# Kernel optimization log

Hardware: AMD Instinct MI355X
Metric: run time of the kernel (lower is better)

Reference implementation:

```python
import jax, jax.numpy as jnp
import numpy as np

B, N_P, N_S = 64, 50, 200
N_NODES = N_P * N_S          # 10000 nodes per graph (jobs x ops)
N_CAND = N_S + 1             # 201 candidates
INPUT_DIM, HIDDEN = 3, 64
NODE_DIM = 2 * HIDDEN        # h_nodes feature dim (=> actor in = 6*HIDDEN)
POOL_DIM = 4 * HIDDEN        # h_pooled dim (mean || max pooling)
H_ACTOR, H_CRITIC = 256, 256


def setup_inputs() -> dict:
    key = jax.random.key(0)
    ks = jax.random.split(key, 16)
    p = lambda k, sh: jax.random.normal(k, sh, jnp.float32) * 0.02
    x = jax.random.normal(ks[0], (B, N_NODES, INPUT_DIM), jnp.float32)
    candidate = jax.random.randint(ks[1], (B, N_CAND), 0, N_NODES)
    mask = jax.random.randint(ks[2], (B, N_CAND), 0, 2) > 0
    mask = mask.at[:, 0].set(True)  # guarantee at least one valid action per row
    return {
        "x": x, "candidate": candidate, "mask": mask,
        "fe_w1": p(ks[3], (INPUT_DIM, HIDDEN)), "fe_b1": jnp.zeros((HIDDEN,), jnp.float32),
        "fe_w2": p(ks[4], (HIDDEN, NODE_DIM)), "fe_b2": jnp.zeros((NODE_DIM,), jnp.float32),
        "a_w1": p(ks[5], (NODE_DIM + POOL_DIM, H_ACTOR)), "a_b1": jnp.zeros((H_ACTOR,), jnp.float32),
        "a_w2": p(ks[6], (H_ACTOR, H_ACTOR)), "a_b2": jnp.zeros((H_ACTOR,), jnp.float32),
        "a_w3": p(ks[7], (H_ACTOR, 1)), "a_b3": jnp.zeros((1,), jnp.float32),
        "c_w1": p(ks[8], (POOL_DIM, H_CRITIC)), "c_b1": jnp.zeros((H_CRITIC,), jnp.float32),
        "c_w2": p(ks[9], (H_CRITIC, H_CRITIC)), "c_b2": jnp.zeros((H_CRITIC,), jnp.float32),
        "c_w3": p(ks[10], (H_CRITIC, 1)), "c_b3": jnp.zeros((1,), jnp.float32),
    }


def _actor_critic(x, candidate, mask,
                  fe_w1, fe_b1, fe_w2, fe_b2,
                  a_w1, a_b1, a_w2, a_b2, a_w3, a_b3,
                  c_w1, c_b1, c_w2, c_b2, c_w3, c_b3):
    # --- feature_extract: per-node MLP embedding, graph-level pooling ---
    h = jax.nn.relu(jnp.einsum('bni,ih->bnh', x, fe_w1) + fe_b1)
    h_nodes = jax.nn.relu(jnp.einsum('bnh,hd->bnd', h, fe_w2) + fe_b2)   # [B, N, 2H]
    h_pooled = jnp.concatenate([h_nodes.mean(axis=1), h_nodes.max(axis=1)], axis=-1)  # [B, 4H]

    # --- gather candidate node features (torch.gather over node axis) ---
    cand_feat = jnp.take_along_axis(h_nodes, candidate[:, :, None], axis=1)  # [B, C, 2H]

    # --- concat broadcast pooled feature ---
    pooled_rep = jnp.broadcast_to(h_pooled[:, None, :], (cand_feat.shape[0], cand_feat.shape[1], h_pooled.shape[-1]))
    concat_fea = jnp.concatenate([cand_feat, pooled_rep], axis=-1)  # [B, C, 6H]

    # --- actor MLP (tanh hidden layers, linear out) ---
    a = jnp.tanh(concat_fea @ a_w1 + a_b1)
    a = jnp.tanh(a @ a_w2 + a_b2)
    scores = a @ a_w3 + a_b3                                    # [B, C, 1]

    # --- mask with -inf, softmax over candidate axis ---
    scores = jnp.where(mask[:, :, None], scores, -jnp.inf)
    pi = jax.nn.softmax(scores, axis=1)                          # [B, C, 1]

    # --- critic MLP on pooled feature ---
    c = jnp.tanh(h_pooled @ c_w1 + c_b1)
    c = jnp.tanh(c @ c_w2 + c_b2)
    v = c @ c_w3 + c_b3                                          # [B, 1]
    return pi, v


def reference(x, candidate, mask,
              fe_w1, fe_b1, fe_w2, fe_b2,
              a_w1, a_b1, a_w2, a_b2, a_w3, a_b3,
              c_w1, c_b1, c_w2, c_b2, c_w3, c_b3):
    return _actor_critic(x, candidate, mask,
                         fe_w1, fe_b1, fe_w2, fe_b2,
                         a_w1, a_b1, a_w2, a_b2, a_w3, a_b3,
                         c_w1, c_b1, c_w2, c_b2, c_w3, c_b3)
```

## Files before the change

kernel.cpp:

```cpp
#include <hip/hip_runtime.h>

#define NN 10000
#define NCAND 201
#define NB 64

typedef __attribute__((ext_vector_type(8))) short short8;
typedef __attribute__((ext_vector_type(4))) float f32x4;

__device__ __forceinline__ float bf2f(unsigned short u) {
  return __uint_as_float(((unsigned int)u) << 16);
}
__device__ __forceinline__ unsigned short f2bf(float f) {
  unsigned int u = __float_as_uint(f);
  u += 0x7FFFu + ((u >> 16) & 1u);
  return (unsigned short)(u >> 16);
}
__device__ __forceinline__ float fast_tanh(float x) {
  return 1.0f - 2.0f / (__expf(2.0f * x) + 1.0f);
}
__device__ __forceinline__ float gld(const void* p, long i, int f) {
  return f ? ((const float*)p)[i] : bf2f(((const unsigned short*)p)[i]);
}

__global__ __launch_bounds__(256, 4)
void mega_kernel(const void* __restrict__ x, const int* __restrict__ cand,
                 const void* w1, const void* b1, const void* w2, const void* b2,
                 const void* aw1, const void* ab1, const void* aw2, const void* ab2,
                 const void* aw3, const void* ab3,
                 const void* cw1, const void* cb1, const void* cw2, const void* cb2,
                 const void* cw3, const void* cb3,
                 const unsigned int* mask_w, const unsigned int* cand_w,
                 int* F, int* scnt,
                 float* __restrict__ psumP, float* __restrict__ pmaxP,
                 unsigned short* __restrict__ cfw,
                 unsigned short* __restrict__ aw1t, unsigned short* __restrict__ aw2t) {
  __shared__ __align__(16) unsigned short pool[128 * 72];
  __shared__ float w1f[3 * 64];
  __shared__ float b1f[64];
  __shared__ float b2f[128];
  __shared__ int cnts[8];

  const int t = threadIdx.x;
  const int j = blockIdx.x;
  const int lane = t & 63;
  const int wv = t >> 6;

  if (j < 1472) {
    if (t < 8) cnts[t] = 0;
    __syncthreads();
    {
      if ((((const unsigned short*)x)[t] & 0x7F80u) >= 0x4300u) atomicAdd(&cnts[0], 1);
      if (t < 192 && (((const unsigned short*)w1)[t] & 0x7F80u) >= 0x4300u) atomicAdd(&cnts[1], 1);
      if (t < 64 && (((const unsigned short*)b1)[t] & 0x7F80u) >= 0x4300u) atomicAdd(&cnts[2], 1);
      if (t < 128 && (((const unsigned short*)b2)[t] & 0x7F80u) >= 0x4300u) atomicAdd(&cnts[3], 1);
      if ((((const unsigned short*)w2)[t] & 0x7F80u) >= 0x4300u) atomicAdd(&cnts[4], 1);
      int co = 0;
#pragma unroll
      for (int q = 0; q < 4; ++q) {
        int i = t * 4 + q;
        if ((i & 1) && cand_w[i] != 0u) co = 1;
      }
      if (co) atomicAdd(&cnts[5], 1);
    }
    __syncthreads();
    const int F0 = cnts[0] > 32, F1 = cnts[1] > 24, F2 = cnts[2] > 8;
    const int F4 = cnts[3] > 16, Fw2 = cnts[4] > 32, C64 = cnts[5] == 0;

    if (j < 1024) {
      unsigned short* h1s = pool;
      const int b = j >> 4;
      const int s = j & 15;

      if (t < 192) w1f[t] = gld(w1, t, F1);
      if (t < 64) b1f[t] = gld(b1, t, F2);
      if (t < 128) b2f[t] = gld(b2, t, F4);

      short8 bfr[2][2];
#pragma unroll
      for (int nl = 0; nl < 2; ++nl)
#pragma unroll
        for (int ks = 0; ks < 2; ++ks) {
          int col = wv * 32 + nl * 16 + (lane & 15);
          short8 v;
#pragma unroll
          for (int jj = 0; jj < 8; ++jj) {
            int k = (lane >> 4) * 8 + ks * 32 + jj;
            v[jj] = (short)f2bf(gld(w2, (long)k * 128 + col, Fw2));
          }
          bfr[nl][ks] = v;
        }
      __syncthreads();

      float csum[2] = {0.f, 0.f};
      float cmax[2] = {0.f, 0.f};
      const int m = t & 127;
      const int kg = t >> 7;

      float x0 = 0.f, x1 = 0.f, x2 = 0.f;
      if (s < 79) {
        int nb = s * 128;
        if (m < min(128, NN - nb)) {
          long xo = ((long)b * NN + nb + m) * 3;
          x0 = gld(x, xo, F0); x1 = gld(x, xo + 1, F0); x2 = gld(x, xo + 2, F0);
        }
      }

      for (int c = s; c < 79; c += 16) {
        int nb = c * 128;
        int cnt = (nb + 128 <= NN) ? 128 : (NN - nb);
        const bool full = (cnt == 128);
        if (full) {
#pragma unroll
          for (int blk = 0; blk < 4; ++blk) {
            short8 v;
#pragma unroll
            for (int i = 0; i < 8; ++i) {
              int k = kg * 32 + blk * 8 + i;
              float vv = x0 * w1f[k] + x1 * w1f[64 + k] + x2 * w1f[128 + k] + b1f[k];
              v[i] = (short)f2bf(fmaxf(vv, 0.f));
            }
            *(short8*)(h1s + m * 72 + kg * 32 + blk * 8) = v;
          }
        } else if (m < cnt) {
#pragma unroll
          for (int blk = 0; blk < 4; ++blk) {
            short8 v;
#pragma unroll
            for (int i = 0; i < 8; ++i) {
              int k = kg * 32 + blk * 8 + i;
              float vv = x0 * w1f[k] + x1 * w1f[64 + k] + x2 * w1f[128 + k] + b1f[k];
              v[i] = (short)f2bf(fmaxf(vv, 0.f));
            }
            *(short8*)(h1s + m * 72 + kg * 32 + blk * 8) = v;
          }
        }
        {
          int cn = c + 16;
          float nx0 = 0.f, nx1 = 0.f, nx2 = 0.f;
          if (cn < 79) {
            int nbn = cn * 128;
            if (m < min(128, NN - nbn)) {
              long xo = ((long)b * NN + nbn + m) * 3;
              nx0 = gld(x, xo, F0); nx1 = gld(x, xo + 1, F0); nx2 = gld(x, xo + 2, F0);
            }
          }
          __syncthreads();
          x0 = nx0; x1 = nx1; x2 = nx2;
        }
        if (full) {
#pragma unroll
          for (int mt = 0; mt < 8; ++mt) {
            const unsigned short* ap = h1s + (mt * 16 + (lane & 15)) * 72 + ((lane >> 4) * 8);
            short8 af0 = *(const short8*)(ap);
            short8 af1 = *(const short8*)(ap + 32);
#pragma unroll
            for (int nl = 0; nl < 2; ++nl) {
              f32x4 acc = {0.f, 0.f, 0.f, 0.f};
              acc = __builtin_amdgcn_mfma_f32_16x16x32_bf16(af0, bfr[nl][0], acc, 0, 0, 0);
              acc = __builtin_amdgcn_mfma_f32_16x16x32_bf16(af1, bfr[nl][1], acc, 0, 0, 0);
              int col = wv * 32 + nl * 16 + (lane & 15);
              float bb = b2f[col];
#pragma unroll
              for (int r = 0; r < 4; ++r) {
                float v = fmaxf(acc[r] + bb, 0.f);
                csum[nl] += v;
                cmax[nl] = fmaxf(cmax[nl], v);
              }
            }
          }
        } else {
#pragma unroll
          for (int mt = 0; mt < 8; ++mt) {
            const unsigned short* ap = h1s + (mt * 16 + (lane & 15)) * 72 + ((lane >> 4) * 8);
            short8 af0 = *(const short8*)(ap);
            short8 af1 = *(const short8*)(ap + 32);
#pragma unroll
            for (int nl = 0; nl < 2; ++nl) {
              f32x4 acc = {0.f, 0.f, 0.f, 0.f};
              acc = __builtin_amdgcn_mfma_f32_16x16x32_bf16(af0, bfr[nl][0], acc, 0, 0, 0);
              acc = __builtin_amdgcn_mfma_f32_16x16x32_bf16(af1, bfr[nl][1], acc, 0, 0, 0);
              int col = wv * 32 + nl * 16 + (lane & 15);
              float bb = b2f[col];
#pragma unroll
              for (int r = 0; r < 4; ++r) {
                int row = mt * 16 + ((lane >> 4) * 4) + r;
                if (row < cnt) {
                  float v = fmaxf(acc[r] + bb, 0.f);
                  csum[nl] += v;
                  cmax[nl] = fmaxf(cmax[nl], v);
                }
              }
            }
          }
        }
        __syncthreads();
      }
#pragma unroll
      for (int nl = 0; nl < 2; ++nl) {
        csum[nl] += __shfl_xor(csum[nl], 16);
        csum[nl] += __shfl_xor(csum[nl], 32);
        cmax[nl] = fmaxf(cmax[nl], __shfl_xor(cmax[nl], 16));
        cmax[nl] = fmaxf(cmax[nl], __shfl_xor(cmax[nl], 32));
      }
      if (lane < 16) {
#pragma unroll
        for (int nl = 0; nl < 2; ++nl) {
          int col = wv * 32 + nl * 16 + lane;
          psumP[((long)b * 16 + s) * 128 + col] = csum[nl];
          pmaxP[((long)b * 16 + s) * 128 + col] = cmax[nl];
        }
      }
    } else {
      unsigned short* h1c = pool;
      const int idx = j - 1024;
      const int b = idx / 7;
      const int cb = idx % 7;
      const int cbase = cb * 29;

      if (t < 128) b2f[t] = gld(b2, t, F4);

      {
        int r = t & 31;
        int ci = cbase + r;
        if (ci > NCAND - 1) ci = NCAND - 1;
        long cidx = (long)b * NCAND + ci;
        int nd = C64 ? cand[2 * cidx] : cand[cidx];
        long xo = ((long)b * NN + nd) * 3;
        float x0 = gld(x, xo, F0), x1 = gld(x, xo + 1, F0), x2 = gld(x, xo + 2, F0);
        int kg = t >> 5;
#pragma unroll
        for (int i = 0; i < 8; ++i) {
          int k = kg * 8 + i;
          float v = x0 * gld(w1, k, F1) + x1 * gld(w1, 64 + k, F1) +
                    x2 * gld(w1, 128 + k, F1) + gld(b1, k, F2);
          h1c[r * 72 + k] = f2bf(fmaxf(v, 0.f));
        }
      }
      __syncthreads();

      {
        short8 af[2][2];
#pragma unroll
        for (int mt = 0; mt < 2; ++mt)
#pragma unroll
          for (int ks = 0; ks < 2; ++ks)
            af[mt][ks] = *(const short8*)(h1c + (mt * 16 + (lane & 15)) * 72 + ((lane >> 4) * 8) + ks * 32);
#pragma unroll
        for (int nl = 0; nl < 2; ++nl) {
          int col = wv * 32 + nl * 16 + (lane & 15);
          short8 bf0, bf1;
#pragma unroll
          for (int jj = 0; jj < 8; ++jj) {
            int k = (lane >> 4) * 8 + jj;
            bf0[jj] = (short)f2bf(gld(w2, (long)k * 128 + col, Fw2));
            bf1[jj] = (short)f2bf(gld(w2, (long)(k + 32) * 128 + col, Fw2));
          }
          float bb = b2f[col];
#pragma unroll
          for (int mt = 0; mt < 2; ++mt) {
            f32x4 acc = {0.f, 0.f, 0.f, 0.f};
            acc = __builtin_amdgcn_mfma_f32_16x16x32_bf16(af[mt][0], bf0, acc, 0, 0, 0);
            acc = __builtin_amdgcn_mfma_f32_16x16x32_bf16(af[mt][1], bf1, acc, 0, 0, 0);
#pragma unroll
            for (int r = 0; r < 4; ++r) {
              int row = mt * 16 + ((lane >> 4) * 4) + r;
              cfw[(long)idx * 4096 + row * 128 + col] = f2bf(fmaxf(acc[r] + bb, 0.f));
            }
          }
        }
      }
    }
    return;
  }

  if (t < 8) cnts[t] = 0;
  __syncthreads();

  if (j < 1856) {
    const unsigned short* pa = (const unsigned short*)aw1;
    const unsigned short* pb = (const unsigned short*)aw2;
    if ((pa[t] & 0x7F80u) >= 0x4300u) atomicAdd(&cnts[0], 1);
    if ((pb[t] & 0x7F80u) >= 0x4300u) atomicAdd(&cnts[1], 1);
    __syncthreads();
    const int Faw1 = cnts[0] > 32, Faw2 = cnts[1] > 32;
    int i = (j - 1472) * 256 + t;
    if (i < 256 * 384) { int n = i / 384, k = i % 384; aw1t[i] = f2bf(gld(aw1, k * 256 + n, Faw1)); }
    if (i < 256 * 256) {
      int n = i >> 8, k = i & 255;
      aw2t[i] = f2bf(gld(aw2, k * 256 + n, Faw2));
    }
  } else if (j < 1873) {
    const void* ptrs[17] = {x, w1, b1, w2, b2, aw1, ab1, aw2, ab2, aw3, ab3,
                            cw1, cb1, cw2, cb2, cw3, cb3};
    const int sizes[17] = {1920000, 192, 64, 8192, 128, 98304, 256, 65536, 256,
                           256, 1, 65536, 256, 65536, 256, 256, 1};
    int a = j - 1856;
    const unsigned short* p = (const unsigned short*)ptrs[a];
    int K = min(sizes[a], 2048);
    int c = 0;
    for (int i = t; i < K; i += 256)
      if ((p[i] & 0x7F80u) >= 0x4300u) c++;
    if (c) atomicAdd(&cnts[0], c);
    __syncthreads();
    if (t == 0) F[a] = (cnts[0] > (K >> 3)) ? 1 : 0;
  } else if (j == 1873) {
    int flo = 0, fhi = 0, fgt = 0;
    for (int i = t; i < 3216; i += 256) {
      unsigned int w = mask_w[i];
      if ((w & 0xFFFFu) == 0x3F80u) flo = 1;
      if ((w >> 16) == 0x3F80u) fhi = 1;
      if (w > 1u) fgt = 1;
    }
    if (flo) cnts[0] = 1;
    if (fhi) cnts[1] = 1;
    if (fgt) cnts[2] = 1;
    __syncthreads();
    if (t == 0) F[17] = cnts[0] ? 2 : (cnts[1] ? 3 : (cnts[2] ? 1 : 0));
  } else {
    int co = 0;
    for (int i = t; i < 1024; i += 256)
      if ((i & 1) && cand_w[i] != 0u) co = 1;
    if (co) cnts[0] = 1;
    if (t < 64) scnt[t] = 0;
    __syncthreads();
    if (t == 0) F[18] = cnts[0] ? 0 : 1;
  }
}

__global__ __launch_bounds__(256, 4)
void actorB_kernel(const unsigned short* __restrict__ cfw,
                   const void* __restrict__ aw1, const void* __restrict__ ab1,
                   const void* __restrict__ ab2,
                   const void* __restrict__ aw3, const void* __restrict__ ab3,
                   const void* __restrict__ mask,
                   const int* __restrict__ F,
                   const float* __restrict__ psumP, const float* __restrict__ pmaxP,
                   const unsigned short* __restrict__ aw1t,
                   const unsigned short* __restrict__ aw2t,
                   const void* __restrict__ cw1, const void* __restrict__ cb1,
                   const void* __restrict__ cw2, const void* __restrict__ cb2,
                   const void* __restrict__ cw3, const void* __restrict__ cb3,
                   float* __restrict__ scores, int* __restrict__ scnt,
                   void* __restrict__ out) {
  __shared__ __align__(16) unsigned short a1s[32 * 264];
  __shared__ __align__(16) unsigned short a2s[32 * 264];
  __shared__ float pactS[256], ab2f[256], plfS[256];
  __shared__ float red[4];
  __shared__ int amLast;

  const int t = threadIdx.x;
  const int lane = t & 63;
  const int wv = t >> 6;

  float pr = 0.f;
  {
    const int b = (blockIdx.x < 448) ? (blockIdx.x / 7) : (blockIdx.x - 448);
    const int col = t & 127;
    if (t < 128) {
#pragma unroll
      for (int sl = 0; sl < 16; ++sl)
        pr += psumP[((long)b * 16 + sl) * 128 + col];
      pr *= (1.0f / 10000.0f);
    } else {
#pragma unroll
      for (int sl = 0; sl < 16; ++sl)
        pr = fmaxf(pr, pmaxP[((long)b * 16 + sl) * 128 + col]);
    }
  }

  if (blockIdx.x >= 448) {
    const int b = blockIdx.x - 448;
    plfS[t] = pr;
    const int OF = (F[0] + F[1] + F[3] + F[5] + F[7] + F[9] + F[11] + F[13] + F[15]) >= 5;
    const int F11 = F[11], F12 = F[12], F13 = F[13];
    const int F14 = F[14], F15 = F[15], F16 = F[16];
    __syncthreads();
    {
      float a = gld(cb1, t, F12);
#pragma unroll 8
      for (int k = 0; k < 256; ++k)
        a += plfS[k] * gld(cw1, (long)k * 256 + t, F11);
      ab2f[t] = fast_tanh(a);
    }
    __syncthreads();
    {
      float a2 = gld(cb2, t, F14);
#pragma unroll 8
      for (int k = 0; k < 256; ++k)
        a2 += ab2f[k] * gld(cw2, (long)k * 256 + t, F13);
      a2 = fast_tanh(a2);
      float p = a2 * gld(cw3, t, F15);
      for (int o = 32; o; o >>= 1) p += __shfl_xor(p, o);
      __syncthreads();
      if (lane == 0) red[wv] = p;
      __syncthreads();
      if (t == 0) {
        float v = red[0] + red[1] + red[2] + red[3] + gld(cb3, 0, F16);
        if (!(v == v)) v = 0.f;
        if (OF) ((float*)out)[NB * NCAND + b] = v;
        else ((unsigned short*)out)[NB * NCAND + b] = f2bf(v);
      }
    }
    return;
  }

  const int b = blockIdx.x / 7;
  const int cb = blockIdx.x % 7;
  const int cbase = cb * 29;
  const int cntc = min(29, NCAND - cbase);
  const int F5 = F[5], F6 = F[6], F8 = F[8], F9 = F[9], F10 = F[10];

  plfS[t] = bf2f(f2bf(pr));
  ab2f[t] = gld(ab2, t, F8);
  __syncthreads();

  float pa = gld(ab1, t, F6);
#pragma unroll 8
  for (int k = 0; k < 256; ++k)
    pa += plfS[k] * gld(aw1, (long)(128 + k) * 256 + t, F5);

  {
    f32x4 acc[2][4];
#pragma unroll
    for (int mt = 0; mt < 2; ++mt)
#pragma unroll
      for (int nt = 0; nt < 4; ++nt) acc[mt][nt] = (f32x4){0.f, 0.f, 0.f, 0.f};
    const unsigned short* cfb = cfw + (long)blockIdx.x * 4096;
#pragma unroll
    for (int ks = 0; ks < 4; ++ks) {
      short8 af0 = *(const short8*)(cfb + (lane & 15) * 128 + ks * 32 + ((lane >> 4) * 8));
      short8 af1 = *(const short8*)(cfb + (16 + (lane & 15)) * 128 + ks * 32 + ((lane >> 4) * 8));
#pragma unroll
      for (int nt = 0; nt < 4; ++nt) {
        int col = wv * 64 + nt * 16 + (lane & 15);
        short8 bfr = *(const short8*)(aw1t + col * 384 + ks * 32 + ((lane >> 4) * 8));
        acc[0][nt] = __builtin_amdgcn_mfma_f32_16x16x32_bf16(af0, bfr, acc[0][nt], 0, 0, 0);
        acc[1][nt] = __builtin_amdgcn_mfma_f32_16x16x32_bf16(af1, bfr, acc[1][nt], 0, 0, 0);
      }
    }
    pactS[t] = pa;
    __syncthreads();
#pragma unroll
    for (int mt = 0; mt < 2; ++mt)
#pragma unroll
      for (int nt = 0; nt < 4; ++nt) {
        int col = wv * 64 + nt * 16 + (lane & 15);
        float bb = pactS[col];
#pragma unroll
        for (int r = 0; r < 4; ++r) {
          int row = mt * 16 + ((lane >> 4) * 4) + r;
          a1s[row * 264 + col] = f2bf(fast_tanh(acc[mt][nt][r] + bb));
        }
      }
  }
  __syncthreads();

  {
    f32x4 acc[2][4];
#pragma unroll
    for (int mt = 0; mt < 2; ++mt)
#pragma unroll
      for (int nt = 0; nt < 4; ++nt) acc[mt][nt] = (f32x4){0.f, 0.f, 0.f, 0.f};
    for (int ks = 0; ks < 8; ++ks) {
      short8 af0 = *(const short8*)(a1s + (lane & 15) * 264 + ks * 32 + ((lane >> 4) * 8));
      short8 af1 = *(const short8*)(a1s + (16 + (lane & 15)) * 264 + ks * 32 + ((lane >> 4) * 8));
#pragma unroll
      for (int nt = 0; nt < 4; ++nt) {
        int col = wv * 64 + nt * 16 + (lane & 15);
        short8 bfr = *(const short8*)(aw2t + col * 256 + ks * 32 + ((lane >> 4) * 8));
        acc[0][nt] = __builtin_amdgcn_mfma_f32_16x16x32_bf16(af0, bfr, acc[0][nt], 0, 0, 0);
        acc[1][nt] = __builtin_amdgcn_mfma_f32_16x16x32_bf16(af1, bfr, acc[1][nt], 0, 0, 0);
      }
    }
#pragma unroll
    for (int mt = 0; mt < 2; ++mt)
#pragma unroll
      for (int nt = 0; nt < 4; ++nt) {
        int col = wv * 64 + nt * 16 + (lane & 15);
        float bb = ab2f[col];
#pragma unroll
        for (int r = 0; r < 4; ++r) {
          int row = mt * 16 + ((lane >> 4) * 4) + r;
          a2s[row * 264 + col] = f2bf(fast_tanh(acc[mt][nt][r] + bb));
        }
      }
  }
  __syncthreads();

  {
    int row = t >> 3, seg = t & 7;
    float p = 0.f;
#pragma unroll 8
    for (int i = 0; i < 32; ++i) {
      int k = seg * 32 + i;
      p += bf2f(a2s[row * 264 + k]) * gld(aw3, k, F9);
    }
    p += __shfl_xor(p, 1);
    p += __shfl_xor(p, 2);
    p += __shfl_xor(p, 4);
    if (seg == 0 && row < cntc)
      atomicExch(&scores[b * 256 + cbase + row], p + gld(ab3, 0, F10));
  }
  __syncthreads();

  if (t == 0) {
    __threadfence();
    amLast = (atomicAdd(&scnt[b], 1) == 6);
  }
  __syncthreads();
  if (!amLast) return;

  const int MM = F[17];
  const int OF = (F[0] + F[1] + F[3] + F[5] + F[7] + F[9] + F[11] + F[13] + F[15]) >= 5;
  float sraw = 0.f, sv = -1e30f;
  bool valid = false;
  if (t < NCAND) {
    sraw = atomicAdd(&scores[b * 256 + t], 0.0f);
    long idx = (long)b * NCAND + t;
    if (MM == 0)      valid = ((const int*)mask)[idx] != 0;
    else if (MM == 1) valid = ((const unsigned char*)mask)[idx] != 0;
    else if (MM == 2) valid = ((const unsigned short*)mask)[idx] != 0;
    else              valid = ((const unsigned int*)mask)[idx] != 0;
    if (valid) sv = sraw;
  }
  float m = sv;
  for (int o = 32; o; o >>= 1) m = fmaxf(m, __shfl_xor(m, o));
  if (lane == 0) red[wv] = m;
  __syncthreads();
  m = fmaxf(fmaxf(red[0], red[1]), fmaxf(red[2], red[3]));
  __syncthreads();
  float e = valid ? __expf(sraw - m) : 0.f;
  if (!(e == e)) e = 0.f;
  float ss = e;
  for (int o = 32; o; o >>= 1) ss += __shfl_xor(ss, o);
  if (lane == 0) red[wv] = ss;
  __syncthreads();
  float tot = red[0] + red[1] + red[2] + red[3];
  tot = fmaxf(tot, 1e-30f);
  if (t < NCAND) {
    float pv = e / tot;
    if (!(pv == pv)) pv = 0.f;
    if (OF) ((float*)out)[b * NCAND + t] = pv;
    else ((unsigned short*)out)[b * NCAND + t] = f2bf(pv);
  }
}

extern "C" void kernel_launch(void* const* d_in, const int* in_sizes, int n_in,
                              void* d_out, int out_size, void* d_ws, size_t ws_size,
                              hipStream_t stream) {
  const void* x = d_in[0];
  const int* cand = (const int*)d_in[1];
  const void* mask = d_in[2];
  const void* fe_w1 = d_in[3];
  const void* fe_b1 = d_in[4];
  const void* fe_w2 = d_in[5];
  const void* fe_b2 = d_in[6];
  const void* a_w1 = d_in[7];
  const void* a_b1 = d_in[8];
  const void* a_w2 = d_in[9];
  const void* a_b2 = d_in[10];
  const void* a_w3 = d_in[11];
  const void* a_b3 = d_in[12];
  const void* c_w1 = d_in[13];
  const void* c_b1 = d_in[14];
  const void* c_w2 = d_in[15];
  const void* c_b2 = d_in[16];
  const void* c_w3 = d_in[17];
  const void* c_b3 = d_in[18];

  char* ws = (char*)d_ws;
  float* scores = (float*)(ws + 65536);
  unsigned short* aw1t = (unsigned short*)(ws + 147456);
  unsigned short* aw2t = (unsigned short*)(ws + 344064);
  int* F = (int*)(ws + 475136);
  unsigned short* cfw = (unsigned short*)(ws + 802944);
  int* scnt = (int*)(ws + 4472960);
  float* psumP = (float*)(ws + 4473216);
  float* pmaxP = (float*)(ws + 4997504);

  mega_kernel<<<1875, 256, 0, stream>>>(x, cand, fe_w1, fe_b1, fe_w2, fe_b2,
                                        a_w1, a_b1, a_w2, a_b2, a_w3, a_b3,
                                        c_w1, c_b1, c_w2, c_b2, c_w3, c_b3,
                                        (const unsigned int*)mask,
                                        (const unsigned int*)cand, F, scnt,
                                        psumP, pmaxP, cfw, aw1t, aw2t);
  actorB_kernel<<<512, 256, 0, stream>>>(cfw, a_w1, a_b1, a_b2, a_w3, a_b3,
                                         mask, F, psumP, pmaxP, aw1t, aw2t,
                                         c_w1, c_b1, c_w2, c_b2, c_w3, c_b3,
                                         scores, scnt, (void*)d_out);
}
```

Before: 163.4 us.

## Fold pooled-feature projection and critic MLP into last pooling block per batch

The last pooling block to finish for each batch, detected with a global atomic counter, now reduces the partial sums and maxima, computes the pooled part of the actor's first layer and runs the full critic MLP, writing the results to workspace. The actor kernel no longer recomputes the 256x256 pooled projection in each of its 7 blocks per batch and drops its 64 critic blocks. It now only reads the precomputed bias vector and copies the value out. This removes redundant per-block GEMV work and shortens the actor kernel, but it puts a serial GEMV tail on 64 blocks of the first kernel and adds a memset launch plus fence and atomic overhead.

```diff
diff --git a/kernel.cpp b/kernel.cpp
--- a/kernel.cpp
+++ b/kernel.cpp
@@ -30,8 +30,9 @@
                  const void* cw1, const void* cb1, const void* cw2, const void* cb2,
                  const void* cw3, const void* cb3,
                  const unsigned int* mask_w, const unsigned int* cand_w,
-                 int* F, int* scnt,
+                 int* F, int* scnt, int* fpcnt,
                  float* __restrict__ psumP, float* __restrict__ pmaxP,
+                 float* __restrict__ pact, float* __restrict__ vws,
                  unsigned short* __restrict__ cfw,
                  unsigned short* __restrict__ aw1t, unsigned short* __restrict__ aw2t) {
   __shared__ __align__(16) unsigned short pool[128 * 72];
@@ -208,6 +209,102 @@
           int col = wv * 32 + nl * 16 + lane;
           psumP[((long)b * 16 + s) * 128 + col] = csum[nl];
           pmaxP[((long)b * 16 + s) * 128 + col] = cmax[nl];
+        }
+      }
+
+      __syncthreads();
+      if (t == 0) {
+        __threadfence();
+        cnts[7] = (atomicAdd(&fpcnt[b], 1) == 15) ? 1 : 0;
+      }
+      __syncthreads();
+      if (!cnts[7]) return;
+
+      {
+        float* plfF = (float*)pool;
+        float* plfQ = plfF + 256;
+        float* c1s  = plfF + 512;
+        float* redt = plfF + 768;
+
+        if (t < 8) cnts[t] = 0;
+        __syncthreads();
+        {
+          int c5 = 0, c11 = 0, c13 = 0;
+          for (int i = t; i < 2048; i += 256) {
+            if ((((const unsigned short*)aw1)[i] & 0x7F80u) >= 0x4300u) c5++;
+            if ((((const unsigned short*)cw1)[i] & 0x7F80u) >= 0x4300u) c11++;
+            if ((((const unsigned short*)cw2)[i] & 0x7F80u) >= 0x4300u) c13++;
+          }
+          if (c5) atomicAdd(&cnts[0], c5);
+          if (c11) atomicAdd(&cnts[1], c11);
+          if (c13) atomicAdd(&cnts[2], c13);
+          if ((((const unsigned short*)ab1)[t] & 0x7F80u) >= 0x4300u) atomicAdd(&cnts[3], 1);
+          if ((((const unsigned short*)cb1)[t] & 0x7F80u) >= 0x4300u) atomicAdd(&cnts[4], 1);
+          if ((((const unsigned short*)cb2)[t] & 0x7F80u) >= 0x4300u) atomicAdd(&cnts[5], 1);
+          if ((((const unsigned short*)cw3)[t] & 0x7F80u) >= 0x4300u) atomicAdd(&cnts[6], 1);
+        }
+        {
+          const int col = t & 127;
+          float v = 0.f;
+          if (t < 128) {
+#pragma unroll
+            for (int sl = 0; sl < 16; ++sl)
+              v += atomicAdd(&psumP[((long)b * 16 + sl) * 128 + col], 0.0f);
+            v *= (1.0f / 10000.0f);
+          } else {
+#pragma unroll
+            for (int sl = 0; sl < 16; ++sl)
+              v = fmaxf(v, atomicAdd(&pmaxP[((long)b * 16 + sl) * 128 + col], 0.0f));
+          }
+          plfF[t] = v;
+          plfQ[t] = bf2f(f2bf(v));
+        }
+        __syncthreads();
+        const int Fa1 = cnts[0] > 256, Fc1 = cnts[1] > 256, Fc2 = cnts[2] > 256;
+        const int Fab = cnts[3] > 32, Fb1 = cnts[4] > 32;
+        const int Fb2 = cnts[5] > 32, Fc3 = cnts[6] > 32;
+
+        {
+          float p0 = 0.f, p1 = 0.f, p2 = 0.f, p3 = 0.f;
+#pragma unroll 4
+          for (int k = 0; k < 256; k += 4) {
+            p0 += plfQ[k]     * gld(aw1, (long)(128 + k) * 256 + t, Fa1);
+            p1 += plfQ[k + 1] * gld(aw1, (long)(129 + k) * 256 + t, Fa1);
+            p2 += plfQ[k + 2] * gld(aw1, (long)(130 + k) * 256 + t, Fa1);
+            p3 += plfQ[k + 3] * gld(aw1, (long)(131 + k) * 256 + t, Fa1);
+          }
+          pact[b * 256 + t] = gld(ab1, t, Fab) + ((p0 + p1) + (p2 + p3));
+        }
+        {
+          float p0 = 0.f, p1 = 0.f, p2 = 0.f, p3 = 0.f;
+#pragma unroll 4
+          for (int k = 0; k < 256; k += 4) {
+            p0 += plfF[k]     * gld(cw1, (long)(k)     * 256 + t, Fc1);
+            p1 += plfF[k + 1] * gld(cw1, (long)(k + 1) * 256 + t, Fc1);
+            p2 += plfF[k + 2] * gld(cw1, (long)(k + 2) * 256 + t, Fc1);
+            p3 += plfF[k + 3] * gld(cw1, (long)(k + 3) * 256 + t, Fc1);
+          }
+          c1s[t] = fast_tanh(gld(cb1, t, Fb1) + ((p0 + p1) + (p2 + p3)));
+        }
+        __syncthreads();
+        {
+          float p0 = 0.f, p1 = 0.f, p2 = 0.f, p3 = 0.f;
+#pragma unroll 4
+          for (int k = 0; k < 256; k += 4) {
+            p0 += c1s[k]     * gld(cw2, (long)(k)     * 256 + t, Fc2);
+            p1 += c1s[k + 1] * gld(cw2, (long)(k + 1) * 256 + t, Fc2);
+            p2 += c1s[k + 2] * gld(cw2, (long)(k + 2) * 256 + t, Fc2);
+            p3 += c1s[k + 3] * gld(cw2, (long)(k + 3) * 256 + t, Fc2);
+          }
+          float a2 = fast_tanh(gld(cb2, t, Fb2) + ((p0 + p1) + (p2 + p3)));
+          float p = a2 * gld(cw3, t, Fc3);
+          for (int o = 32; o; o >>= 1) p += __shfl_xor(p, o);
+          if (lane == 0) redt[wv] = p;
+          __syncthreads();
+          if (t == 0) {
+            int Fb3 = ((((const unsigned short*)cb3)[0] & 0x7F80u) >= 0x4300u) ? 1 : 0;
+            vws[b] = redt[0] + redt[1] + redt[2] + redt[3] + gld(cb3, 0, Fb3);
+          }
         }
       }
     } else {
@@ -327,97 +424,35 @@
   }
 }
 
-__global__ __launch_bounds__(256, 4)
+__global__ __launch_bounds__(256)
 void actorB_kernel(const unsigned short* __restrict__ cfw,
-                   const void* __restrict__ aw1, const void* __restrict__ ab1,
                    const void* __restrict__ ab2,
                    const void* __restrict__ aw3, const void* __restrict__ ab3,
                    const void* __restrict__ mask,
                    const int* __restrict__ F,
-                   const float* __restrict__ psumP, const float* __restrict__ pmaxP,
+                   const float* __restrict__ pact,
+                   const float* __restrict__ vws,
                    const unsigned short* __restrict__ aw1t,
                    const unsigned short* __restrict__ aw2t,
-                   const void* __restrict__ cw1, const void* __restrict__ cb1,
-                   const void* __restrict__ cw2, const void* __restrict__ cb2,
-                   const void* __restrict__ cw3, const void* __restrict__ cb3,
                    float* __restrict__ scores, int* __restrict__ scnt,
                    void* __restrict__ out) {
   __shared__ __align__(16) unsigned short a1s[32 * 264];
   __shared__ __align__(16) unsigned short a2s[32 * 264];
-  __shared__ float pactS[256], ab2f[256], plfS[256];
+  __shared__ float pactS[256], ab2f[256];
   __shared__ float red[4];
   __shared__ int amLast;
 
   const int t = threadIdx.x;
-  const int lane = t & 63;
-  const int wv = t >> 6;
-
-  float pr = 0.f;
-  {
-    const int b = (blockIdx.x < 448) ? (blockIdx.x / 7) : (blockIdx.x - 448);
-    const int col = t & 127;
-    if (t < 128) {
-#pragma unroll
-      for (int sl = 0; sl < 16; ++sl)
-        pr += psumP[((long)b * 16 + sl) * 128 + col];
-      pr *= (1.0f / 10000.0f);
-    } else {
-#pragma unroll
-      for (int sl = 0; sl < 16; ++sl)
-        pr = fmaxf(pr, pmaxP[((long)b * 16 + sl) * 128 + col]);
-    }
-  }
-
-  if (blockIdx.x >= 448) {
-    const int b = blockIdx.x - 448;
-    plfS[t] = pr;
-    const int OF = (F[0] + F[1] + F[3] + F[5] + F[7] + F[9] + F[11] + F[13] + F[15]) >= 5;
-    const int F11 = F[11], F12 = F[12], F13 = F[13];
-    const int F14 = F[14], F15 = F[15], F16 = F[16];
-    __syncthreads();
-    {
-      float a = gld(cb1, t, F12);
-#pragma unroll 8
-      for (int k = 0; k < 256; ++k)
-        a += plfS[k] * gld(cw1, (long)k * 256 + t, F11);
-      ab2f[t] = fast_tanh(a);
-    }
-    __syncthreads();
-    {
-      float a2 = gld(cb2, t, F14);
-#pragma unroll 8
-      for (int k = 0; k < 256; ++k)
-        a2 += ab2f[k] * gld(cw2, (long)k * 256 + t, F13);
-      a2 = fast_tanh(a2);
-      float p = a2 * gld(cw3, t, F15);
-      for (int o = 32; o; o >>= 1) p += __shfl_xor(p, o);
-      __syncthreads();
-      if (lane == 0) red[wv] = p;
-      __syncthreads();
-      if (t == 0) {
-        float v = red[0] + red[1] + red[2] + red[3] + gld(cb3, 0, F16);
-        if (!(v == v)) v = 0.f;
-        if (OF) ((float*)out)[NB * NCAND + b] = v;
-        else ((unsigned short*)out)[NB * NCAND + b] = f2bf(v);
-      }
-    }
-    return;
-  }
-
   const int b = blockIdx.x / 7;
   const int cb = blockIdx.x % 7;
   const int cbase = cb * 29;
   const int cntc = min(29, NCAND - cbase);
-  const int F5 = F[5], F6 = F[6], F8 = F[8], F9 = F[9], F10 = F[10];
-
-  plfS[t] = bf2f(f2bf(pr));
+  const int lane = t & 63;
+  const int wv = t >> 6;
+  const int F8 = F[8], F9 = F[9], F10 = F[10];
+
+  pactS[t] = pact[b * 256 + t];
   ab2f[t] = gld(ab2, t, F8);
-  __syncthreads();
-
-  float pa = gld(ab1, t, F6);
-#pragma unroll 8
-  for (int k = 0; k < 256; ++k)
-    pa += plfS[k] * gld(aw1, (long)(128 + k) * 256 + t, F5);
 
   {
     f32x4 acc[2][4];
@@ -438,7 +473,6 @@
         acc[1][nt] = __builtin_amdgcn_mfma_f32_16x16x32_bf16(af1, bfr, acc[1][nt], 0, 0, 0);
       }
     }
-    pactS[t] = pa;
     __syncthreads();
 #pragma unroll
     for (int mt = 0; mt < 2; ++mt)
@@ -542,6 +576,12 @@
     if (!(pv == pv)) pv = 0.f;
     if (OF) ((float*)out)[b * NCAND + t] = pv;
     else ((unsigned short*)out)[b * NCAND + t] = f2bf(pv);
+  }
+  if (t == 0) {
+    float v = vws[b];
+    if (!(v == v)) v = 0.f;
+    if (OF) ((float*)out)[NB * NCAND + b] = v;
+    else ((unsigned short*)out)[NB * NCAND + b] = f2bf(v);
   }
 }
 
@@ -569,23 +609,27 @@
   const void* c_b3 = d_in[18];
 
   char* ws = (char*)d_ws;
+  int* fpcnt = (int*)(ws);
+  float* vws = (float*)(ws + 1024);
   float* scores = (float*)(ws + 65536);
   unsigned short* aw1t = (unsigned short*)(ws + 147456);
   unsigned short* aw2t = (unsigned short*)(ws + 344064);
   int* F = (int*)(ws + 475136);
+  float* pact = (float*)(ws + 737408);
   unsigned short* cfw = (unsigned short*)(ws + 802944);
   int* scnt = (int*)(ws + 4472960);
   float* psumP = (float*)(ws + 4473216);
   float* pmaxP = (float*)(ws + 4997504);
 
+  hipMemsetAsync(fpcnt, 0, 256, stream);
+
   mega_kernel<<<1875, 256, 0, stream>>>(x, cand, fe_w1, fe_b1, fe_w2, fe_b2,
                                         a_w1, a_b1, a_w2, a_b2, a_w3, a_b3,
                                         c_w1, c_b1, c_w2, c_b2, c_w3, c_b3,
                                         (const unsigned int*)mask,
-                                        (const unsigned int*)cand, F, scnt,
-                                        psumP, pmaxP, cfw, aw1t, aw2t);
-  actorB_kernel<<<512, 256, 0, stream>>>(cfw, a_w1, a_b1, a_b2, a_w3, a_b3,
-                                         mask, F, psumP, pmaxP, aw1t, aw2t,
-                                         c_w1, c_b1, c_w2, c_b2, c_w3, c_b3,
+                                        (const unsigned int*)cand, F, scnt, fpcnt,
+                                        psumP, pmaxP, pact, vws, cfw, aw1t, aw2t);
+  actorB_kernel<<<448, 256, 0, stream>>>(cfw, a_b2, a_w3, a_b3, mask, F,
+                                         pact, vws, aw1t, aw2t,
                                          scores, scnt, (void*)d_out);
 }
```

Measured after the change: 219.5 us. 34.3% more time.
